# Kernel optimization log

Hardware: AMD Instinct MI355X
Metric: run time of the kernel (lower is better)

The kernel has to match this reference:

```python
import jax, jax.numpy as jnp
import numpy as np

DIM = 512; HEADS = 8; DH = 64; M = 256; ITERS = 6; RK = 33; NCLS = 2

def _ln(x, g, b, eps=1e-5):
    mu = x.mean(-1, keepdims=True)
    var = ((x - mu) ** 2).mean(-1, keepdims=True)
    return (x - mu) * jax.lax.rsqrt(var + eps) * g + b

def _dwconv(x, w, b=None):
    # x: [B,C,H,W], w: [C,1,kh,kw], depthwise (groups=C)
    kh, kw = w.shape[2], w.shape[3]
    y = jax.lax.conv_general_dilated(x, w, (1, 1), [(kh // 2, kh // 2), (kw // 2, kw // 2)],
                                     feature_group_count=x.shape[1],
                                     dimension_numbers=('NCHW', 'OIHW', 'NCHW'))
    if b is not None:
        y = y + b[None, :, None, None]
    return y

def _pinv(x):
    # Moore-Penrose iterative pseudo-inverse (lucidrains nystrom-attention)
    denom = jnp.max(jnp.abs(x).sum(-1)) * jnp.max(jnp.abs(x).sum(-2))
    z = jnp.swapaxes(x, -1, -2) / denom
    I = jnp.eye(x.shape[-1], dtype=x.dtype)
    for _ in range(ITERS):
        xz = x @ z
        z = 0.25 * z @ (13 * I - xz @ (15 * I - xz @ (7 * I - xz)))
    return z

def _nystrom(x, qkv_w, out_w, out_b, res_w):
    b, n, _ = x.shape
    pad = (-n) % M  # front-pad so seq divisible by num_landmarks
    xp = jnp.pad(x, ((0, 0), (pad, 0), (0, 0)))
    q, k, v = jnp.split(xp @ qkv_w, 3, axis=-1)
    heads = lambda t: t.reshape(b, -1, HEADS, DH).transpose(0, 2, 1, 3)  # [b,h,np,d]
    q, k, v = heads(q), heads(k), heads(v)
    q = q * (DH ** -0.5)
    l = (n + pad) // M
    ql = q.reshape(b, HEADS, M, l, DH).mean(3)  # [b,h,m,d]
    kl = k.reshape(b, HEADS, M, l, DH).mean(3)
    a1 = jax.nn.softmax(jnp.einsum('bhid,bhjd->bhij', q, kl), -1)   # [b,h,np,m]
    a2 = jax.nn.softmax(jnp.einsum('bhid,bhjd->bhij', ql, kl), -1)  # [b,h,m,m]
    a3 = jax.nn.softmax(jnp.einsum('bhid,bhjd->bhij', ql, k), -1)   # [b,h,m,np]
    out = (a1 @ _pinv(a2)) @ (a3 @ v)
    # residual depthwise conv over sequence per head: v as [B,C=h,H=np,W=d]
    out = out + jax.lax.conv_general_dilated(v, res_w, (1, 1), [(RK // 2, RK // 2), (0, 0)],
                                             feature_group_count=HEADS,
                                             dimension_numbers=('NCHW', 'OIHW', 'NCHW'))
    out = out.transpose(0, 2, 1, 3).reshape(b, -1, HEADS * DH)
    return (out @ out_w + out_b)[:, -n:]

def _translayer(x, ng, nb, qkv_w, out_w, out_b, res_w):
    x = _ln(x, ng, nb)
    return x + _nystrom(x, qkv_w, out_w, out_b, res_w)

def _ppeg(x, H, W, w7, b7, w5, b5, w3, b3):
    B, _, C = x.shape
    cls, feat = x[:, 0], x[:, 1:]
    f = feat.transpose(0, 2, 1).reshape(B, C, H, W)
    y = _dwconv(f, w7, b7) + f + _dwconv(f, w5, b5) + _dwconv(f, w3, b3)
    y = y.reshape(B, C, H * W).transpose(0, 2, 1)
    return jnp.concatenate([cls[:, None], y], 1)

def setup_inputs() -> dict:
    key = jax.random.key(0)
    ks = jax.random.split(key, 20)
    B, N, F = 1, 10000, 1024
    s = 0.02
    d = {}
    d['h'] = jax.random.normal(ks[0], (B, N, F), jnp.float32)
    d['fc1_w'] = jax.random.normal(ks[1], (F, DIM)) * s
    d['fc1_b'] = jnp.zeros((DIM,))
    d['cls_token'] = jax.random.normal(ks[2], (1, 1, DIM))
    for i, p in enumerate(['l1', 'l2']):
        d[p + '_norm_g'] = jnp.ones((DIM,)); d[p + '_norm_b'] = jnp.zeros((DIM,))
        d[p + '_qkv_w'] = jax.random.normal(ks[3 + 3 * i], (DIM, 3 * DIM)) * s
        d[p + '_out_w'] = jax.random.normal(ks[4 + 3 * i], (DIM, DIM)) * s
        d[p + '_out_b'] = jnp.zeros((DIM,))
        d[p + '_res_w'] = jax.random.normal(ks[5 + 3 * i], (HEADS, 1, RK, 1)) * s
    for j, kk in enumerate([7, 5, 3]):
        d['ppeg_w%d' % kk] = jax.random.normal(ks[10 + j], (DIM, 1, kk, kk)) * s
        d['ppeg_b%d' % kk] = jnp.zeros((DIM,))
    d['norm_g'] = jnp.ones((DIM,)); d['norm_b'] = jnp.zeros((DIM,))
    d['fc2_w'] = jax.random.normal(ks[15], (DIM, NCLS)) * s
    d['fc2_b'] = jnp.zeros((NCLS,))
    return d

def reference(h, fc1_w, fc1_b, cls_token,
              l1_norm_g, l1_norm_b, l1_qkv_w, l1_out_w, l1_out_b, l1_res_w,
              ppeg_w7, ppeg_b7, ppeg_w5, ppeg_b5, ppeg_w3, ppeg_b3,
              l2_norm_g, l2_norm_b, l2_qkv_w, l2_out_w, l2_out_b, l2_res_w,
              norm_g, norm_b, fc2_w, fc2_b):
    h = jax.nn.relu(h @ fc1_w + fc1_b)
    N = h.shape[1]
    sq = int(np.ceil(np.sqrt(N)))
    add = sq * sq - N
    h = jnp.concatenate([h, h[:, :add]], 1)
    cls = jnp.broadcast_to(cls_token, (h.shape[0], 1, DIM)).astype(h.dtype)
    h = jnp.concatenate([cls, h], 1)
    h = _translayer(h, l1_norm_g, l1_norm_b, l1_qkv_w, l1_out_w, l1_out_b, l1_res_w)
    h = _ppeg(h, sq, sq, ppeg_w7, ppeg_b7, ppeg_w5, ppeg_b5, ppeg_w3, ppeg_b3)
    h = _translayer(h, l2_norm_g, l2_norm_b, l2_qkv_w, l2_out_w, l2_out_b, l2_res_w)
    h = _ln(h, norm_g, norm_b)[:, 0]
    return h @ fc2_w + fc2_b
```

## Files before the change

### kernel.cpp

```cpp
#include <hip/hip_runtime.h>
#include <math.h>

#define LPAD  10240
#define NSEQ  10001
#define PADT  239
#define NPIX  10000

typedef unsigned short u16;
typedef __attribute__((ext_vector_type(8))) short short8;
typedef __attribute__((ext_vector_type(4))) float floatx4;

__device__ __forceinline__ float b2f(u16 u){ return __uint_as_float(((unsigned)u)<<16); }
__device__ __forceinline__ u16 f2b(float f){
    unsigned x = __float_as_uint(f);
    return (u16)((x + 0x7FFFu + ((x>>16)&1u)) >> 16);
}
__device__ __forceinline__ void gld16(const void* g, void* l){
    __builtin_amdgcn_global_load_lds(
        (const __attribute__((address_space(1))) unsigned int*)g,
        (__attribute__((address_space(3))) unsigned int*)l, 16, 0, 0);
}

__global__ __launch_bounds__(256) void gemm_mfma(
    const u16* __restrict__ A, int lda, long sA,
    const u16* __restrict__ Bt, int ldb, long sB,
    void* __restrict__ Cv, int ldc, long sC,
    int M, int N, int K, int ksplit,
    const float* __restrict__ bias,
    const float* __restrict__ resid, int ldr,
    int relu, int qscale, int obf16, int atomic)
{
    __shared__ u16 As[2][64*32];
    __shared__ u16 Bs[2][128*32];

    int bz = blockIdx.z / ksplit;
    int ks = blockIdx.z - bz * ksplit;
    A  += (size_t)bz * sA;
    Bt += (size_t)bz * sB;

    int kchunk = (K + ksplit - 1) / ksplit;
    kchunk = (kchunk + 31) & ~31;
    int kbeg = ks * kchunk;
    int kend = kbeg + kchunk; if (kend > K) kend = K;

    int tid = threadIdx.x;
    int w = tid >> 6, lane = tid & 63;
    int wm = (w >> 1) * 32, wn = (w & 1) * 64;
    int m0 = blockIdx.y * 64, n0 = blockIdx.x * 128;

    int l4 = lane >> 2;
    int lk = (lane & 3) * 8;
    int ra = w * 16 + l4;
    int rb = w * 32 + l4;
    int am0 = m0 + ra;      if (am0 > M-1) am0 = M-1;
    int bn0 = n0 + rb;      if (bn0 > N-1) bn0 = N-1;
    int bn1 = n0 + rb + 16; if (bn1 > N-1) bn1 = N-1;
    const u16* ag0 = A  + (size_t)am0 * lda + lk;
    const u16* bg0 = Bt + (size_t)bn0 * ldb + lk;
    const u16* bg1 = Bt + (size_t)bn1 * ldb + lk;
    int soA  = w * 512;
    int soB0 = w * 1024;
    int soB1 = w * 1024 + 512;

    floatx4 acc[2][4];
    #pragma unroll
    for (int i = 0; i < 2; i++)
        #pragma unroll
        for (int j = 0; j < 4; j++)
            acc[i][j] = (floatx4){0.f, 0.f, 0.f, 0.f};

    int arow = wm + (lane & 15);
    int nrow = wn + (lane & 15);
    int koff = (lane >> 4) * 8;

    if (kbeg < kend) {
        gld16(ag0 + kbeg, &As[0][soA]);
        gld16(bg0 + kbeg, &Bs[0][soB0]);
        gld16(bg1 + kbeg, &Bs[0][soB1]);
    }
    __syncthreads();

    int cb = 0;
    for (int k0 = kbeg; k0 < kend; k0 += 32) {
        int kn = k0 + 32;
        if (kn < kend) {
            gld16(ag0 + kn, &As[cb ^ 1][soA]);
            gld16(bg0 + kn, &Bs[cb ^ 1][soB0]);
            gld16(bg1 + kn, &Bs[cb ^ 1][soB1]);
        }
        short8 af[2], bf[4];
        #pragma unroll
        for (int i = 0; i < 2; i++) af[i] = *(const short8*)&As[cb][(arow + i*16)*32 + koff];
        #pragma unroll
        for (int j = 0; j < 4; j++) bf[j] = *(const short8*)&Bs[cb][(nrow + j*16)*32 + koff];
        #pragma unroll
        for (int i = 0; i < 2; i++)
            #pragma unroll
            for (int j = 0; j < 4; j++)
                acc[i][j] = __builtin_amdgcn_mfma_f32_16x16x32_bf16(af[i], bf[j], acc[i][j], 0, 0, 0);
        __syncthreads();
        cb ^= 1;
    }

    float* Cf = (float*)Cv;
    u16*   Ch = (u16*)Cv;
    size_t cb2 = (size_t)bz * sC;
    int rbase = m0 + wm + (lane >> 4) * 4;
    int cbase = n0 + wn + (lane & 15);
    #pragma unroll
    for (int i = 0; i < 2; i++) {
        #pragma unroll
        for (int j = 0; j < 4; j++) {
            int col = cbase + j * 16;
            if (col >= N) continue;
            float bcol = bias ? bias[col] : 0.f;
            #pragma unroll
            for (int r = 0; r < 4; r++) {
                int row = rbase + i * 16 + r;
                if (row >= M) continue;
                float v = acc[i][j][r];
                if (qscale && col < 512) v *= 0.125f;
                v += bcol;
                if (resid) v += resid[(size_t)row * ldr + col];
                if (relu) v = fmaxf(v, 0.f);
                size_t ci = cb2 + (size_t)row * ldc + col;
                if (obf16) Ch[ci] = f2b(v);
                else if (atomic) atomicAdd(&Cf[ci], v);
                else Cf[ci] = v;
            }
        }
    }
}

__global__ __launch_bounds__(256) void gemm_big(
    const float* __restrict__ A, int lda, long sA,
    const float* __restrict__ B, int ldb, long sB,
    float* __restrict__ C, int ldc, long sC,
    int M, int N, int K,
    float alpha, float diagc,
    const float* __restrict__ bias,
    const float* __restrict__ resid, int ldr, long sR, float rescoef,
    int btrans)
{
    __shared__ float As[2][16][20];
    __shared__ float Bs[2][16][64];

    int bz = blockIdx.z;
    A += (size_t)bz * sA;
    B += (size_t)bz * sB;
    C += (size_t)bz * sC;

    int tid = threadIdx.x;
    int tx = tid & 15, ty = tid >> 4;
    int m0 = blockIdx.y * 16, n0 = blockIdx.x * 64;

    int ar = tid >> 2;
    int ak = (tid & 3) * 4;
    int bkr = tid >> 4;
    int bc4 = (tid & 15) * 4;
    int bc  = tid >> 2;
    int bkq = (tid & 3) * 4;

    auto loadA = [&](int k0, float4& ra) {
        if (tid < 64) {
            int m = m0 + ar;
            ra = make_float4(0.f, 0.f, 0.f, 0.f);
            if (m < M) ra = *(const float4*)(A + (size_t)m * lda + k0 + ak);
        }
    };
    auto loadB = [&](int k0, float4& rb) {
        if (!btrans) rb = *(const float4*)(B + (size_t)(k0 + bkr) * ldb + n0 + bc4);
        else         rb = *(const float4*)(B + (size_t)(n0 + bc) * ldb + k0 + bkq);
    };
    auto storeA = [&](int buf, const float4& ra) {
        if (tid < 64) {
            As[buf][ak + 0][ar] = ra.x; As[buf][ak + 1][ar] = ra.y;
            As[buf][ak + 2][ar] = ra.z; As[buf][ak + 3][ar] = ra.w;
        }
    };
    auto storeB = [&](int buf, const float4& rb) {
        if (!btrans) {
            *(float4*)&Bs[buf][bkr][bc4] = rb;
        } else {
            Bs[buf][bkq + 0][bc] = rb.x; Bs[buf][bkq + 1][bc] = rb.y;
            Bs[buf][bkq + 2][bc] = rb.z; Bs[buf][bkq + 3][bc] = rb.w;
        }
    };

    float acc[4];
    #pragma unroll
    for (int j = 0; j < 4; j++) acc[j] = 0.f;

    float4 pa, pb;
    loadA(0, pa); loadB(0, pb);
    storeA(0, pa); storeB(0, pb);
    int cur = 0;

    for (int k0 = 0; k0 < K; k0 += 16) {
        bool more = (k0 + 16) < K;
        float4 na, nb;
        if (more) { loadA(k0 + 16, na); loadB(k0 + 16, nb); }
        __syncthreads();
        #pragma unroll
        for (int k = 0; k < 16; k++) {
            float a = As[cur][k][ty];
            float4 bv = *(const float4*)&Bs[cur][k][tx * 4];
            acc[0] += a * bv.x; acc[1] += a * bv.y;
            acc[2] += a * bv.z; acc[3] += a * bv.w;
        }
        if (more) { storeA(cur ^ 1, na); storeB(cur ^ 1, nb); cur ^= 1; }
    }

    int m = m0 + ty;
    if (m < M) {
        #pragma unroll
        for (int j = 0; j < 4; j++) {
            int n = n0 + tx * 4 + j;
            float v = alpha * acc[j];
            if (diagc != 0.f && m == n) v += diagc;
            if (bias) v += bias[n];
            if (resid) v += rescoef * resid[(size_t)bz * sR + (size_t)m * ldr + n];
            C[(size_t)m * ldc + n] = v;
        }
    }
}

__global__ __launch_bounds__(256, 2) void a1z_fused(
    const u16* __restrict__ QKVh, const u16* __restrict__ KLh,
    const u16* __restrict__ ZTh, float* __restrict__ OUT, int T0)
{
    __shared__ u16 Ps[64 * 264];

    int tid = threadIdx.x;
    int w = tid >> 6, lane = tid & 63;
    int lo = lane & 15, hi = lane >> 4;
    int koff = hi * 8;
    int hh = blockIdx.y;
    int tok0 = T0 + blockIdx.x * 64;

    int trow = tok0 + w * 16 + lo;
    if (trow > LPAD - 1) trow = LPAD - 1;

    const u16* qb = QKVh + (size_t)trow * 1536 + hh * 64 + koff;
    short8 aq0 = *(const short8*)(qb);
    short8 aq1 = *(const short8*)(qb + 32);

    floatx4 acc[16];
    #pragma unroll
    for (int j = 0; j < 16; j++) acc[j] = (floatx4){0.f, 0.f, 0.f, 0.f};

    const u16* klb = KLh + (size_t)hh * 256 * 64 + lo * 64 + koff;
    {
        short8 bk[16];
        #pragma unroll
        for (int j = 0; j < 16; j++) bk[j] = *(const short8*)(klb + (size_t)j * 1024);
        #pragma unroll
        for (int j = 0; j < 16; j++)
            acc[j] = __builtin_amdgcn_mfma_f32_16x16x32_bf16(aq0, bk[j], acc[j], 0, 0, 0);
    }
    {
        short8 bk[16];
        #pragma unroll
        for (int j = 0; j < 16; j++) bk[j] = *(const short8*)(klb + (size_t)j * 1024 + 32);
        #pragma unroll
        for (int j = 0; j < 16; j++)
            acc[j] = __builtin_amdgcn_mfma_f32_16x16x32_bf16(aq1, bk[j], acc[j], 0, 0, 0);
    }

    #pragma unroll
    for (int slot = 0; slot < 4; slot++) {
        float mx = acc[0][slot];
        #pragma unroll
        for (int j = 1; j < 16; j++) mx = fmaxf(mx, acc[j][slot]);
        mx = fmaxf(mx, __shfl_xor(mx, 1, 64));
        mx = fmaxf(mx, __shfl_xor(mx, 2, 64));
        mx = fmaxf(mx, __shfl_xor(mx, 4, 64));
        mx = fmaxf(mx, __shfl_xor(mx, 8, 64));
        float p[16];
        float s = 0.f;
        #pragma unroll
        for (int j = 0; j < 16; j++) { p[j] = __expf(acc[j][slot] - mx); s += p[j]; }
        s += __shfl_xor(s, 1, 64);
        s += __shfl_xor(s, 2, 64);
        s += __shfl_xor(s, 4, 64);
        s += __shfl_xor(s, 8, 64);
        float inv = 1.f / s;
        int row = w * 16 + hi * 4 + slot;
        #pragma unroll
        for (int j = 0; j < 16; j++)
            Ps[row * 264 + j * 16 + lo] = f2b(p[j] * inv);
    }

    floatx4 acc2[4];
    #pragma unroll
    for (int j = 0; j < 4; j++) acc2[j] = (floatx4){0.f, 0.f, 0.f, 0.f};
    const u16* ztb = ZTh + ((size_t)hh * 64 + lo) * 256 + koff;
    #pragma unroll
    for (int ks = 0; ks < 8; ks++) {
        short8 bz[4];
        #pragma unroll
        for (int j = 0; j < 4; j++)
            bz[j] = *(const short8*)(ztb + (size_t)j * 4096 + ks * 32);
        short8 ap = *(const short8*)&Ps[(w * 16 + lo) * 264 + ks * 32 + koff];
        #pragma unroll
        for (int j = 0; j < 4; j++)
            acc2[j] = __builtin_amdgcn_mfma_f32_16x16x32_bf16(ap, bz[j], acc2[j], 0, 0, 0);
    }
    #pragma unroll
    for (int j = 0; j < 4; j++) {
        #pragma unroll
        for (int slot = 0; slot < 4; slot++) {
            int tok = tok0 + w * 16 + hi * 4 + slot;
            if (tok < LPAD)
                OUT[(size_t)tok * 512 + hh * 64 + j * 16 + lo] = acc2[j][slot];
        }
    }
}

__global__ __launch_bounds__(256) void ln_kernel(
    const float* __restrict__ X, float* __restrict__ OUT, u16* __restrict__ OUTH,
    const float* __restrict__ g, const float* __restrict__ b, int nrows)
{
    int row = blockIdx.x * 4 + (threadIdx.x >> 6);
    int lane = threadIdx.x & 63;
    if (row >= nrows) return;
    const float* xr = X + (size_t)row * 512;
    float v[8]; float s = 0.f, s2 = 0.f;
    #pragma unroll
    for (int i = 0; i < 8; i++) { float t = xr[lane + i * 64]; v[i] = t; s += t; s2 += t * t; }
    for (int o = 1; o < 64; o <<= 1) { s += __shfl_xor(s, o, 64); s2 += __shfl_xor(s2, o, 64); }
    float mu = s * (1.f / 512.f);
    float var = s2 * (1.f / 512.f) - mu * mu;
    float rs = rsqrtf(var + 1e-5f);
    float* orow = OUT + (size_t)row * 512;
    u16* hrow = OUTH + (size_t)row * 512;
    #pragma unroll
    for (int i = 0; i < 8; i++) {
        int j = lane + i * 64;
        float y = (v[i] - mu) * rs * g[j] + b[j];
        orow[j] = y;
        hrow[j] = f2b(y);
    }
}

__global__ __launch_bounds__(64) void landmarks_kernel(
    const u16* __restrict__ QKVh, float* __restrict__ QL, float* __restrict__ KL,
    u16* __restrict__ QLh, u16* __restrict__ KLh)
{
    int mm = blockIdx.x, hh = blockIdx.y;
    int d = threadIdx.x;
    const u16* base = QKVh + (size_t)(mm * 40) * 1536 + hh * 64 + d;
    float sq = 0.f, sk = 0.f;
    for (int li = 0; li < 40; li++) {
        sq += b2f(base[(size_t)li * 1536]);
        sk += b2f(base[(size_t)li * 1536 + 512]);
    }
    size_t o = ((size_t)hh * 256 + mm) * 64 + d;
    float q = sq * (1.f / 40.f), k = sk * (1.f / 40.f);
    QL[o] = q; KL[o] = k;
    QLh[o] = f2b(q); KLh[o] = f2b(k);
}

__global__ __launch_bounds__(256) void softmax_a2(
    float* __restrict__ A2, int nrows)
{
    int row = blockIdx.x * 4 + (threadIdx.x >> 6);
    int lane = threadIdx.x & 63;
    if (row >= nrows) return;
    float* p = A2 + (size_t)row * 256 + lane * 4;
    float4 v = *(float4*)p;
    float mx = fmaxf(fmaxf(v.x, v.y), fmaxf(v.z, v.w));
    for (int o = 1; o < 64; o <<= 1) mx = fmaxf(mx, __shfl_xor(mx, o, 64));
    float4 e = make_float4(__expf(v.x - mx), __expf(v.y - mx),
                           __expf(v.z - mx), __expf(v.w - mx));
    float s = e.x + e.y + e.z + e.w;
    for (int o = 1; o < 64; o <<= 1) s += __shfl_xor(s, o, 64);
    float inv = 1.f / s;
    e.x *= inv; e.y *= inv; e.z *= inv; e.w *= inv;
    *(float4*)p = e;
}

__global__ __launch_bounds__(256) void row_softmax_bf16(
    const float* __restrict__ S, u16* __restrict__ P, int ncols)
{
    int row = blockIdx.x;
    const float* p = S + (size_t)row * ncols;
    u16* q = P + (size_t)row * ncols;
    int tid = threadIdx.x;
    __shared__ float sr1[4], sr2[4];
    float mx = -1e30f;
    for (int i = tid; i < ncols; i += 256) mx = fmaxf(mx, p[i]);
    for (int o = 1; o < 64; o <<= 1) mx = fmaxf(mx, __shfl_xor(mx, o, 64));
    if ((tid & 63) == 0) sr1[tid >> 6] = mx;
    __syncthreads();
    mx = fmaxf(fmaxf(sr1[0], sr1[1]), fmaxf(sr1[2], sr1[3]));
    float s = 0.f;
    for (int i = tid; i < ncols; i += 256) s += __expf(p[i] - mx);
    for (int o = 1; o < 64; o <<= 1) s += __shfl_xor(s, o, 64);
    if ((tid & 63) == 0) sr2[tid >> 6] = s;
    __syncthreads();
    s = sr2[0] + sr2[1] + sr2[2] + sr2[3];
    float inv = 1.f / s;
    for (int i = tid; i < ncols; i += 256) q[i] = f2b(__expf(p[i] - mx) * inv);
}

__global__ __launch_bounds__(256) void a2norms_kernel(
    const float* __restrict__ A2, float* __restrict__ scal)
{
    int hh = blockIdx.x, tid = threadIdx.x;
    const float* A = A2 + (size_t)hh * 65536;
    float rs = 0.f, cs = 0.f;
    for (int j = 0; j < 256; j++) {
        rs += fabsf(A[(size_t)tid * 256 + j]);
        cs += fabsf(A[(size_t)j * 256 + tid]);
    }
    __shared__ float sm[8];
    for (int o = 1; o < 64; o <<= 1) {
        rs = fmaxf(rs, __shfl_xor(rs, o, 64));
        cs = fmaxf(cs, __shfl_xor(cs, o, 64));
    }
    if ((tid & 63) == 0) { sm[tid >> 6] = rs; sm[4 + (tid >> 6)] = cs; }
    __syncthreads();
    if (tid == 0) {
        float rm = fmaxf(fmaxf(sm[0], sm[1]), fmaxf(sm[2], sm[3]));
        float cm = fmaxf(fmaxf(sm[4], sm[5]), fmaxf(sm[6], sm[7]));
        atomicMax((unsigned int*)&scal[0], __float_as_uint(rm));
        atomicMax((unsigned int*)&scal[1], __float_as_uint(cm));
    }
}

__global__ __launch_bounds__(256) void z0_kernel(
    const float* __restrict__ A2, const float* __restrict__ scal,
    float* __restrict__ Zf)
{
    int i = blockIdx.x, hh = blockIdx.y, j = threadIdx.x;
    float inv = 1.f / (scal[0] * scal[1]);
    Zf[((size_t)hh * 256 + i) * 256 + j] = A2[((size_t)hh * 256 + j) * 256 + i] * inv;
}

__global__ __launch_bounds__(256) void a1z_single(
    const u16* __restrict__ QKVh, const float* __restrict__ KL,
    const float* __restrict__ ZM, float* __restrict__ OUT, int tok)
{
    int h = blockIdx.x, tid = threadIdx.x;
    __shared__ float q[64];
    __shared__ float p[256];
    __shared__ float red[4];
    if (tid < 64) q[tid] = b2f(QKVh[(size_t)tok * 1536 + h * 64 + tid]);
    __syncthreads();
    const float* kl = KL + ((size_t)h * 256 + tid) * 64;
    float s = 0.f;
    for (int d = 0; d < 64; d++) s += q[d] * kl[d];
    float mx = s;
    for (int o = 1; o < 64; o <<= 1) mx = fmaxf(mx, __shfl_xor(mx, o, 64));
    if ((tid & 63) == 0) red[tid >> 6] = mx;
    __syncthreads();
    mx = fmaxf(fmaxf(red[0], red[1]), fmaxf(red[2], red[3]));
    float e = __expf(s - mx);
    float sum = e;
    for (int o = 1; o < 64; o <<= 1) sum += __shfl_xor(sum, o, 64);
    __syncthreads();
    if ((tid & 63) == 0) red[tid >> 6] = sum;
    __syncthreads();
    sum = red[0] + red[1] + red[2] + red[3];
    p[tid] = e / sum;
    __syncthreads();
    if (tid < 64) {
        float a = 0.f;
        for (int j = 0; j < 256; j++) a += p[j] * ZM[((size_t)h * 256 + j) * 64 + tid];
        OUT[(size_t)tok * 512 + h * 64 + tid] = a;
    }
}

__global__ __launch_bounds__(256) void conv_cast(
    const u16* __restrict__ QKVh, const float* __restrict__ OUT,
    u16* __restrict__ OUTH, const float* __restrict__ resw, int T0, int ntok)
{
    __shared__ u16 Vw[48][512];
    __shared__ float ws[264];
    int tid = threadIdx.x;
    int t0 = T0 + blockIdx.x * 16;
    int wv = tid >> 6, lnn = tid & 63;
    for (int r = wv; r < 48; r += 4) {
        int ts = t0 - 16 + r;
        short8 v = (short8){0,0,0,0,0,0,0,0};
        if (ts >= 0 && ts < LPAD)
            v = *(const short8*)(QKVh + (size_t)ts * 1536 + 1024 + lnn * 8);
        *(short8*)&Vw[r][lnn * 8] = v;
    }
    if (tid < 264) ws[tid] = resw[tid];
    __syncthreads();

    int c0 = tid * 2;
    int h = c0 >> 6;
    float wreg[33];
    #pragma unroll
    for (int r = 0; r < 33; r++) wreg[r] = ws[h * 33 + r];

    #pragma unroll 1
    for (int tk = 0; tk < 16; tk++) {
        int tok = t0 + tk;
        if (tok >= T0 + ntok) break;
        float a0 = 0.f, a1 = 0.f;
        #pragma unroll
        for (int r = 0; r < 33; r++) {
            unsigned pv = *(const unsigned*)&Vw[tk + r][c0];
            a0 += wreg[r] * __uint_as_float(pv << 16);
            a1 += wreg[r] * __uint_as_float(pv & 0xFFFF0000u);
        }
        float v0 = OUT[(size_t)tok * 512 + c0]     + a0;
        float v1 = OUT[(size_t)tok * 512 + c0 + 1] + a1;
        unsigned pk = ((unsigned)f2b(v1) << 16) | (unsigned)f2b(v0);
        *(unsigned*)&OUTH[(size_t)(tok - T0) * 512 + c0] = pk;
    }
}

__global__ __launch_bounds__(256) void conv_res(
    const u16* __restrict__ QKVh, float* __restrict__ OUT,
    const float* __restrict__ resw, int t0, int ntok)
{
    int idx = blockIdx.x * 256 + threadIdx.x;
    if (idx >= ntok * 512) return;
    int tok = t0 + (idx >> 9);
    int c = idx & 511;
    int h = c >> 6;
    const u16* vbase = QKVh + 1024 + c;
    float acc = 0.f;
    #pragma unroll 1
    for (int r = 0; r < 33; r++) {
        int ts = tok - 16 + r;
        if (ts >= 0 && ts < LPAD)
            acc += resw[h * 33 + r] * b2f(vbase[(size_t)ts * 1536]);
    }
    OUT[(size_t)tok * 512 + c] += acc;
}

__global__ __launch_bounds__(256) void vtrans(
    const u16* __restrict__ QKVh, u16* __restrict__ Vt)
{
    int t0 = blockIdx.x * 64, hh = blockIdx.y;
    __shared__ u16 tile[64][65];
    #pragma unroll
    for (int ii = 0; ii < 16; ii++) {
        int idx = threadIdx.x + ii * 256;
        int t = idx >> 6, d = idx & 63;
        tile[t][d] = QKVh[(size_t)(t0 + t) * 1536 + 1024 + hh * 64 + d];
    }
    __syncthreads();
    #pragma unroll
    for (int ii = 0; ii < 16; ii++) {
        int idx = threadIdx.x + ii * 256;
        int d = idx >> 6, t = idx & 63;
        Vt[((size_t)hh * 64 + d) * LPAD + t0 + t] = tile[t][d];
    }
}

__global__ void ppeg_combine(
    const float* __restrict__ w7, const float* __restrict__ w5,
    const float* __restrict__ w3, const float* __restrict__ b7,
    const float* __restrict__ b5, const float* __restrict__ b3,
    float* __restrict__ W49, float* __restrict__ BSUM)
{
    int idx = blockIdx.x * 256 + threadIdx.x;
    if (idx >= 49 * 512) return;
    int tap = idx >> 9, c = idx & 511;
    int dy = tap / 7 - 3, dx = tap % 7 - 3;
    float v = w7[c * 49 + tap];
    if (dy >= -2 && dy <= 2 && dx >= -2 && dx <= 2)
        v += w5[c * 25 + (dy + 2) * 5 + (dx + 2)];
    if (dy >= -1 && dy <= 1 && dx >= -1 && dx <= 1)
        v += w3[c * 9 + (dy + 1) * 3 + (dx + 1)];
    W49[tap * 512 + c] = v;
    if (tap == 0) BSUM[c] = b7[c] + b5[c] + b3[c];
}

__global__ __launch_bounds__(256) void ppeg_tile(
    const float* __restrict__ S, float* __restrict__ O,
    const float* __restrict__ W49, const float* __restrict__ BSUM)
{
    __shared__ float Sw[10][22][64];
    int tid = threadIdx.x;
    int c = tid & 63;
    int sub = tid >> 6;
    int x0 = blockIdx.x * 16;
    int y0 = blockIdx.y * 4;
    int cg = blockIdx.z * 64;

    {
        int p = tid >> 4;
        int c4 = (tid & 15) * 4;
        #pragma unroll
        for (int i = 0; i < 14; i++) {
            int f = p + i * 16;
            if (f < 220) {
                int r = f / 22, xx = f - r * 22;
                int gy = y0 - 3 + r;
                int gx = x0 - 3 + xx;
                float4 v = make_float4(0.f, 0.f, 0.f, 0.f);
                if ((unsigned)gy < 100u && (unsigned)gx < 100u)
                    v = *(const float4*)(S + (size_t)(1 + gy * 100 + gx) * 512 + cg + c4);
                *(float4*)&Sw[r][xx][c4] = v;
            }
        }
    }
    float wreg[49];
    #pragma unroll
    for (int t = 0; t < 49; t++) wreg[t] = W49[t * 512 + cg + c];
    float bsum = BSUM[cg + c];
    __syncthreads();

    int xb = sub * 4;
    float acc[4][4];
    #pragma unroll
    for (int yy = 0; yy < 4; yy++)
        #pragma unroll
        for (int xq = 0; xq < 4; xq++)
            acc[yy][xq] = Sw[yy + 3][xb + xq + 3][c] + bsum;

    #pragma unroll
    for (int r = 0; r < 10; r++) {
        float v[10];
        #pragma unroll
        for (int j = 0; j < 10; j++) v[j] = Sw[r][xb + j][c];
        #pragma unroll
        for (int yy = 0; yy < 4; yy++) {
            int t = r - yy;
            if (t < 0 || t > 6) continue;
            #pragma unroll
            for (int dxt = 0; dxt < 7; dxt++) {
                float w = wreg[t * 7 + dxt];
                #pragma unroll
                for (int xq = 0; xq < 4; xq++)
                    acc[yy][xq] += v[xq + dxt] * w;
            }
        }
    }

    #pragma unroll
    for (int yy = 0; yy < 4; yy++) {
        int gy = y0 + yy;
        #pragma unroll
        for (int xq = 0; xq < 4; xq++) {
            int gx = x0 + xb + xq;
            if (gx < 100)
                O[(size_t)(1 + gy * 100 + gx) * 512 + cg + c] = acc[yy][xq];
        }
    }
}

__global__ __launch_bounds__(64) void final_kernel(
    const float* __restrict__ S, const float* __restrict__ g, const float* __restrict__ b,
    const float* __restrict__ w, const float* __restrict__ bb, float* __restrict__ out)
{
    int lane = threadIdx.x;
    float v[8]; float s = 0.f, s2 = 0.f;
    #pragma unroll
    for (int i = 0; i < 8; i++) { float t = S[lane + i * 64]; v[i] = t; s += t; s2 += t * t; }
    for (int o = 1; o < 64; o <<= 1) { s += __shfl_xor(s, o, 64); s2 += __shfl_xor(s2, o, 64); }
    float mu = s * (1.f / 512.f);
    float var = s2 * (1.f / 512.f) - mu * mu;
    float rs = rsqrtf(var + 1e-5f);
    float o0 = 0.f, o1 = 0.f;
    #pragma unroll
    for (int i = 0; i < 8; i++) {
        int j = lane + i * 64;
        float xn = (v[i] - mu) * rs * g[j] + b[j];
        o0 += xn * w[j * 2 + 0];
        o1 += xn * w[j * 2 + 1];
    }
    for (int o = 1; o < 64; o <<= 1) { o0 += __shfl_xor(o0, o, 64); o1 += __shfl_xor(o1, o, 64); }
    if (lane == 0) { out[0] = o0 + bb[0]; out[1] = o1 + bb[1]; }
}

__global__ void zerok(float* p, int n)
{
    int i = blockIdx.x * 256 + threadIdx.x;
    if (i < n) p[i] = 0.f;
}
__global__ void zero2k(float* p) { p[0] = 0.f; p[1] = 0.f; }
__global__ void copy512(float* dst, const float* src)
{
    int i = blockIdx.x * 256 + threadIdx.x;
    if (i < 512) dst[i] = src[i];
}
__global__ void cast_bf16(const float* __restrict__ src, u16* __restrict__ dst, int n)
{
    int i = (blockIdx.x * 256 + threadIdx.x) * 4;
    if (i >= n) return;
    float4 v = *(const float4*)(src + i);
    dst[i + 0] = f2b(v.x); dst[i + 1] = f2b(v.y);
    dst[i + 2] = f2b(v.z); dst[i + 3] = f2b(v.w);
}
__global__ void castT(const float* __restrict__ src, u16* __restrict__ dst,
                      int R, int C, int nb)
{
    size_t idx = (size_t)blockIdx.x * 256 + threadIdx.x;
    size_t tot = (size_t)R * C * nb;
    if (idx >= tot) return;
    int rc = R * C;
    int b = (int)(idx / rc);
    int rem = (int)(idx - (size_t)b * rc);
    int c = rem / R, r = rem - c * R;
    dst[idx] = f2b(src[(size_t)b * rc + (size_t)r * C + c]);
}

extern "C" void kernel_launch(void* const* d_in, const int* in_sizes, int n_in,
                              void* d_out, int out_size, void* d_ws, size_t ws_size,
                              hipStream_t stream)
{
    const float* h     = (const float*)d_in[0];
    const float* fc1_w = (const float*)d_in[1];
    const float* fc1_b = (const float*)d_in[2];
    const float* cls   = (const float*)d_in[3];
    bool sigorder = (in_sizes[10] == 512 * 49);
    int i_l2 = sigorder ? 16 : 10;
    int i_pp = sigorder ? 10 : 16;
    const float* l_g[2]   = { (const float*)d_in[4], (const float*)d_in[i_l2 + 0] };
    const float* l_b[2]   = { (const float*)d_in[5], (const float*)d_in[i_l2 + 1] };
    const float* l_qkv[2] = { (const float*)d_in[6], (const float*)d_in[i_l2 + 2] };
    const float* l_ow[2]  = { (const float*)d_in[7], (const float*)d_in[i_l2 + 3] };
    const float* l_ob[2]  = { (const float*)d_in[8], (const float*)d_in[i_l2 + 4] };
    const float* l_rw[2]  = { (const float*)d_in[9], (const float*)d_in[i_l2 + 5] };
    const float* w7 = (const float*)d_in[i_pp + 0];
    const float* b7 = (const float*)d_in[i_pp + 1];
    const float* w5 = (const float*)d_in[i_pp + 2];
    const float* b5 = (const float*)d_in[i_pp + 3];
    const float* w3 = (const float*)d_in[i_pp + 4];
    const float* b3 = (const float*)d_in[i_pp + 5];
    const float* ng   = (const float*)d_in[22];
    const float* nbv  = (const float*)d_in[23];
    const float* fc2w = (const float*)d_in[24];
    const float* fc2b = (const float*)d_in[25];
    float* out = (float*)d_out;

    char* Wb = (char*)d_ws;
    size_t off = 0;
    auto allocB = [&](size_t bytes) { void* p = Wb + off; off = (off + bytes + 255) & ~(size_t)255; return p; };

    float* SEQ   = (float*)allocB((size_t)NSEQ * 512 * 4);
    float* XP    = (float*)allocB((size_t)LPAD * 512 * 4);
    u16*   XPh   = (u16*)  allocB((size_t)LPAD * 512 * 2);
    u16*   QKVh  = (u16*)  allocB((size_t)LPAD * 1536 * 2);
    float* QLKL  = (float*)allocB((size_t)262144 * 4);
    float* QL = QLKL, *KL = QLKL + 131072;
    u16*   QLKLh = (u16*)  allocB((size_t)262144 * 2);
    u16*   QLh = QLKLh, *KLh = QLKLh + 131072;
    float* A2   = (float*)allocB(524288 * 4);
    float* Zf0  = (float*)allocB(524288 * 4);
    float* Zf1  = (float*)allocB(524288 * 4);
    float* XZf  = (float*)allocB(524288 * 4);
    float* W2b  = (float*)allocB(524288 * 4);
    float* W3b  = (float*)allocB(524288 * 4);
    float* A3V  = (float*)allocB(131072 * 4);
    float* ZMATf= (float*)allocB(131072 * 4);
    u16*   ZMATt= (u16*)  allocB(131072 * 2);
    u16*   Vt   = (u16*)  allocB((size_t)8 * 64 * LPAD * 2);
    u16*   fc1wt= (u16*)  allocB(524288 * 2);
    u16*   qkvwt= (u16*)  allocB(786432 * 2);
    u16*   outwt= (u16*)  allocB(262144 * 2);
    float* W49  = (float*)allocB(49 * 512 * 4);
    float* BSUM = (float*)allocB(512 * 4);
    float* SCAL = (float*)allocB(16);
    void*  U1   = allocB((size_t)LPAD * 512 * 4);
    u16*   hbf  = (u16*)U1;
    float* OUT  = (float*)U1;
    float* SEQ2 = OUT;
    size_t fixed = off;

    size_t scB_b = (size_t)8 * 256 * LPAD * 4;
    size_t phB_b = (size_t)8 * 256 * LPAD * 2;
    bool batched = ws_size >= fixed + scB_b + phB_b;
    float* SC; u16* Ph;
    if (batched) {
        SC = (float*)(Wb + fixed);
        Ph = (u16*)(Wb + fixed + scB_b);
    } else {
        SC = (float*)(Wb + fixed);
        Ph = (u16*)(Wb + fixed + (size_t)256 * LPAD * 4);
    }
    u16* OUTh = (u16*)SC;

    auto mgemm = [&](const u16* A, int lda, long sA, const u16* Bt, int ldb, long sB,
                     void* C, int ldc, long sC, int M, int N, int K,
                     const float* bias, const float* resid, int ldr,
                     int relu, int qscale, int obf16, int nbatch, int ksplit, int atomic) {
        dim3 grid((N + 127) / 128, (M + 63) / 64, nbatch * ksplit);
        gemm_mfma<<<grid, 256, 0, stream>>>(A, lda, sA, Bt, ldb, sB, C, ldc, sC,
            M, N, K, ksplit, bias, resid, ldr, relu, qscale, obf16, atomic);
    };
    auto fgemm = [&](const float* A, int lda, long sA, const float* B, int ldb, long sB,
                     float* C, int ldc, long sC, int M, int N, int K,
                     float alpha, float diagc, const float* bias,
                     const float* resid, int ldr, long sR, float rescoef,
                     int btrans, int nbatch) {
        dim3 grid(N / 64, (M + 15) / 16, nbatch);
        gemm_big<<<grid, 256, 0, stream>>>(A, lda, sA, B, ldb, sB, C, ldc, sC, M, N, K,
            alpha, diagc, bias, resid, ldr, sR, rescoef, btrans);
    };

    cast_bf16<<<(NPIX * 1024 / 4 + 255) / 256, 256, 0, stream>>>(h, hbf, NPIX * 1024);
    castT<<<(524288 + 255) / 256, 256, 0, stream>>>(fc1_w, fc1wt, 1024, 512, 1);
    mgemm(hbf, 1024, 0, fc1wt, 1024, 0, SEQ + 512, 512, 0, NPIX, 512, 1024,
          fc1_b, nullptr, 0, 1, 0, 0, 1, 1, 0);
    copy512<<<2, 256, 0, stream>>>(SEQ, cls);
    zerok<<<(PADT * 512 + 255) / 256, 256, 0, stream>>>(XP, PADT * 512);
    zerok<<<(PADT * 256 + 255) / 256, 256, 0, stream>>>((float*)XPh, PADT * 256);
    ppeg_combine<<<(49 * 512 + 255) / 256, 256, 0, stream>>>(w7, w5, w3, b7, b5, b3, W49, BSUM);

    for (int layer = 0; layer < 2; layer++) {
        const float* curSEQ = (layer == 0) ? SEQ : SEQ2;
        ln_kernel<<<(NSEQ + 3) / 4, 256, 0, stream>>>(curSEQ, XP + (size_t)PADT * 512,
            XPh + (size_t)PADT * 512, l_g[layer], l_b[layer], NSEQ);
        castT<<<(786432 + 255) / 256, 256, 0, stream>>>(l_qkv[layer], qkvwt, 512, 1536, 1);
        mgemm(XPh, 512, 0, qkvwt, 512, 0, QKVh, 1536, 0, LPAD, 1536, 512,
              nullptr, nullptr, 0, 0, 1, 1, 1, 1, 0);
        landmarks_kernel<<<dim3(256, 8), 64, 0, stream>>>(QKVh, QL, KL, QLh, KLh);
        fgemm(QL, 64, 16384, KL, 64, 16384, A2, 256, 65536, 256, 256, 64,
              1.f, 0.f, nullptr, nullptr, 0, 0, 0.f, 1, 8);
        softmax_a2<<<512, 256, 0, stream>>>(A2, 2048);
        zero2k<<<1, 1, 0, stream>>>(SCAL);
        a2norms_kernel<<<8, 256, 0, stream>>>(A2, SCAL);
        z0_kernel<<<dim3(256, 8), 256, 0, stream>>>(A2, SCAL, Zf0);

        float* zc = Zf0; float* zn = Zf1;
        for (int it = 0; it < 6; it++) {
            fgemm(A2, 256, 65536, zc, 256, 65536, XZf, 256, 65536, 256, 256, 256,
                  1.f, 0.f, nullptr, nullptr, 0, 0, 0.f, 0, 8);
            fgemm(XZf, 256, 65536, XZf, 256, 65536, W2b, 256, 65536, 256, 256, 256,
                  1.f, 15.f, nullptr, XZf, 256, 65536, -7.f, 0, 8);
            fgemm(XZf, 256, 65536, W2b, 256, 65536, W3b, 256, 65536, 256, 256, 256,
                  -1.f, 13.f, nullptr, nullptr, 0, 0, 0.f, 0, 8);
            fgemm(zc, 256, 65536, W3b, 256, 65536, zn, 256, 65536, 256, 256, 256,
                  0.25f, 0.f, nullptr, nullptr, 0, 0, 0.f, 0, 8);
            float* t = zc; zc = zn; zn = t;
        }
        float* zfin = zc;

        vtrans<<<dim3(160, 8), 256, 0, stream>>>(QKVh, Vt);
        zerok<<<512, 256, 0, stream>>>(A3V, 131072);
        if (batched) {
            mgemm(QLh, 64, 16384, QKVh + 512, 1536, 64, SC, LPAD, (long)256 * LPAD,
                  256, LPAD, 64, nullptr, nullptr, 0, 0, 0, 0, 8, 1, 0);
            row_softmax_bf16<<<2048, 256, 0, stream>>>(SC, Ph, LPAD);
            mgemm(Ph, LPAD, (long)256 * LPAD, Vt, LPAD, (long)64 * LPAD, A3V, 64, 16384,
                  256, 64, LPAD, nullptr, nullptr, 0, 0, 0, 0, 8, 40, 1);
        } else {
            for (int hh = 0; hh < 8; hh++) {
                mgemm(QLh + (size_t)hh * 16384, 64, 0, QKVh + 512 + hh * 64, 1536, 0,
                      SC, LPAD, 0, 256, LPAD, 64, nullptr, nullptr, 0, 0, 0, 0, 1, 1, 0);
                row_softmax_bf16<<<256, 256, 0, stream>>>(SC, Ph, LPAD);
                mgemm(Ph, LPAD, 0, Vt + (size_t)hh * 64 * LPAD, LPAD, 0,
                      A3V + (size_t)hh * 16384, 64, 0, 256, 64, LPAD,
                      nullptr, nullptr, 0, 0, 0, 0, 1, 40, 1);
            }
        }
        fgemm(zfin, 256, 65536, A3V, 64, 16384, ZMATf, 64, 16384, 256, 64, 256,
              1.f, 0.f, nullptr, nullptr, 0, 0, 0.f, 0, 8);

        if (layer == 0) {
            castT<<<(131072 + 255) / 256, 256, 0, stream>>>(ZMATf, ZMATt, 256, 64, 8);
            a1z_fused<<<dim3((NSEQ + 63) / 64, 8), 256, 0, stream>>>(
                QKVh, KLh, ZMATt, OUT, PADT);
            conv_cast<<<(NSEQ + 15) / 16, 256, 0, stream>>>(
                QKVh, OUT, OUTh, l_rw[0], PADT, NSEQ);
            castT<<<(262144 + 255) / 256, 256, 0, stream>>>(l_ow[0], outwt, 512, 512, 1);
            mgemm(OUTh, 512, 0, outwt, 512, 0, SEQ, 512, 0, NSEQ, 512, 512,
                  l_ob[0], XP + (size_t)PADT * 512, 512, 0, 0, 0, 1, 1, 0);
            ppeg_tile<<<dim3(7, 25, 8), 256, 0, stream>>>(SEQ, SEQ2, W49, BSUM);
            copy512<<<2, 256, 0, stream>>>(SEQ2, SEQ);
        } else {
            a1z_single<<<8, 256, 0, stream>>>(QKVh, KL, ZMATf, OUT, PADT);
            conv_res<<<2, 256, 0, stream>>>(QKVh, OUT, l_rw[1], PADT, 1);
            fgemm(OUT + (size_t)PADT * 512, 512, 0, l_ow[1], 512, 0, SEQ, 512, 0,
                  1, 512, 512, 1.f, 0.f, l_ob[1],
                  XP + (size_t)PADT * 512, 512, 0, 1.f, 0, 1);
        }
    }
    final_kernel<<<1, 64, 0, stream>>>(SEQ, ng, nbv, fc2w, fc2b, out);
    (void)n_in; (void)out_size;
}
```

Before: 1.549 ms.

## Swizzle GEMM blocks across XCDs, XOR-swizzle LDS k-offsets, vectorize softmax via LDS

The GEMM now remaps workgroup IDs so consecutive tiles land on the same XCD, aiming for better L2 reuse. It also XOR-swizzles the k-chunk offsets used for LDS writes and MFMA fragment reads to cut bank conflicts. The bf16 row softmax caches each row in LDS with float4 loads, so the later passes no longer reread global memory, and it writes packed ushort4 outputs. The risks are that the swizzle must map every element consistently between the load and read sides, the 40KB LDS buffer lowers occupancy, and the float4 accesses assume ncols is a multiple of 4 and the rows are aligned.

New measurement: 1.518 ms. -2.0%, faster.

```diff
diff --git a/kernel.cpp b/kernel.cpp
--- a/kernel.cpp
+++ b/kernel.cpp
@@ -38,6 +38,15 @@
     A  += (size_t)bz * sA;
     Bt += (size_t)bz * sB;
 
+    int gx = gridDim.x, gy = gridDim.y;
+    int nwg = gx * gy;
+    int orig = blockIdx.y * gx + blockIdx.x;
+    int xcd = orig & 7, lin = orig >> 3;
+    int qq = nwg >> 3, rr = nwg & 7;
+    int swz = (xcd < rr) ? (xcd * (qq + 1) + lin)
+                         : (rr * (qq + 1) + (xcd - rr) * qq + lin);
+    int bx = swz % gx, by = swz / gx;
+
     int kchunk = (K + ksplit - 1) / ksplit;
     kchunk = (kchunk + 31) & ~31;
     int kbeg = ks * kchunk;
@@ -46,10 +55,10 @@
     int tid = threadIdx.x;
     int w = tid >> 6, lane = tid & 63;
     int wm = (w >> 1) * 32, wn = (w & 1) * 64;
-    int m0 = blockIdx.y * 64, n0 = blockIdx.x * 128;
+    int m0 = by * 64, n0 = bx * 128;
 
     int l4 = lane >> 2;
-    int lk = (lane & 3) * 8;
+    int lk = (((lane & 3) ^ (l4 & 3)) * 8);
     int ra = w * 16 + l4;
     int rb = w * 32 + l4;
     int am0 = m0 + ra;      if (am0 > M-1) am0 = M-1;
@@ -71,7 +80,7 @@
 
     int arow = wm + (lane & 15);
     int nrow = wn + (lane & 15);
-    int koff = (lane >> 4) * 8;
+    int koff = (((lane >> 4) ^ (lane & 3)) * 8);
 
     if (kbeg < kend) {
         gld16(ag0 + kbeg, &As[0][soA]);
@@ -383,25 +392,45 @@
 __global__ __launch_bounds__(256) void row_softmax_bf16(
     const float* __restrict__ S, u16* __restrict__ P, int ncols)
 {
+    __shared__ float buf[LPAD];
+    __shared__ float sr[4];
     int row = blockIdx.x;
     const float* p = S + (size_t)row * ncols;
     u16* q = P + (size_t)row * ncols;
     int tid = threadIdx.x;
-    __shared__ float sr1[4], sr2[4];
+
     float mx = -1e30f;
-    for (int i = tid; i < ncols; i += 256) mx = fmaxf(mx, p[i]);
+    for (int i = tid * 4; i < ncols; i += 1024) {
+        float4 v = *(const float4*)(p + i);
+        *(float4*)&buf[i] = v;
+        mx = fmaxf(mx, fmaxf(fmaxf(v.x, v.y), fmaxf(v.z, v.w)));
+    }
     for (int o = 1; o < 64; o <<= 1) mx = fmaxf(mx, __shfl_xor(mx, o, 64));
-    if ((tid & 63) == 0) sr1[tid >> 6] = mx;
-    __syncthreads();
-    mx = fmaxf(fmaxf(sr1[0], sr1[1]), fmaxf(sr1[2], sr1[3]));
+    if ((tid & 63) == 0) sr[tid >> 6] = mx;
+    __syncthreads();
+    mx = fmaxf(fmaxf(sr[0], sr[1]), fmaxf(sr[2], sr[3]));
+
     float s = 0.f;
-    for (int i = tid; i < ncols; i += 256) s += __expf(p[i] - mx);
+    for (int i = tid * 4; i < ncols; i += 1024) {
+        float4 v = *(const float4*)&buf[i];
+        s += __expf(v.x - mx) + __expf(v.y - mx) + __expf(v.z - mx) + __expf(v.w - mx);
+    }
     for (int o = 1; o < 64; o <<= 1) s += __shfl_xor(s, o, 64);
-    if ((tid & 63) == 0) sr2[tid >> 6] = s;
-    __syncthreads();
-    s = sr2[0] + sr2[1] + sr2[2] + sr2[3];
+    __syncthreads();
+    if ((tid & 63) == 0) sr[tid >> 6] = s;
+    __syncthreads();
+    s = sr[0] + sr[1] + sr[2] + sr[3];
     float inv = 1.f / s;
-    for (int i = tid; i < ncols; i += 256) q[i] = f2b(__expf(p[i] - mx) * inv);
+
+    for (int i = tid * 4; i < ncols; i += 1024) {
+        float4 v = *(const float4*)&buf[i];
+        ushort4 o4;
+        o4.x = f2b(__expf(v.x - mx) * inv);
+        o4.y = f2b(__expf(v.y - mx) * inv);
+        o4.z = f2b(__expf(v.z - mx) * inv);
+        o4.w = f2b(__expf(v.w - mx) * inv);
+        *(ushort4*)(q + i) = o4;
+    }
 }
 
 __global__ __launch_bounds__(256) void a2norms_kernel(
```
